# Performance work log

Measured on AMD Instinct MI355X. Metric: run time of the kernel, lower is better.

Reference implementation:

```python
import jax, jax.numpy as jnp
import numpy as np

B, C_ADD, H, W, NB = 4, 4, 496, 432, 50
SCALE = 0.8  # nonzero indices are multiplied by 0.8 in the original code


def setup_inputs() -> dict:
    key = jax.random.key(0)
    k1, k2, k3 = jax.random.split(key, 3)
    added_points = jax.random.normal(k1, (B, C_ADD, H, W), dtype=jnp.float32)
    original_points = jax.random.normal(k2, (B, C_ADD + 1, H, W), dtype=jnp.float32)
    # boxes: [x, y, z, dx, dy, dz, heading]; centers inside scaled grid extent
    u = jax.random.uniform(k3, (B, NB, 7), dtype=jnp.float32)
    cx = u[..., 0] * (H * SCALE)
    cy = u[..., 1] * (W * SCALE)
    cz = jnp.zeros_like(cx)
    dx = 2.0 + u[..., 3] * 6.0
    dy = 2.0 + u[..., 4] * 6.0
    dz = 1.0 + u[..., 5] * 2.0
    heading = (u[..., 6] - 0.5) * (2.0 * np.pi)
    boxes = jnp.stack([cx, cy, cz, dx, dy, dz, heading], axis=-1)
    return {"added_points": added_points, "original_points": original_points, "boxes": boxes}


def _points_in_boxes(points, boxes):
    # points: [P, 3]; boxes: [B, Nb, 7] -> bool [B, Nb, P]
    # OpenPCDet-style axis-aligned check in the box's rotated local frame.
    px = points[:, 0][None, None, :] - boxes[..., 0, None]  # [B, Nb, P]
    py = points[:, 1][None, None, :] - boxes[..., 1, None]
    pz = points[:, 2][None, None, :] - boxes[..., 2, None]
    c = jnp.cos(boxes[..., 6])[..., None]
    s = jnp.sin(boxes[..., 6])[..., None]
    lx = px * c + py * s
    ly = -px * s + py * c
    return (
        (jnp.abs(lx) <= boxes[..., 3, None] * 0.5)
        & (jnp.abs(ly) <= boxes[..., 4, None] * 0.5)
        & (jnp.abs(pz) <= boxes[..., 5, None] * 0.5)
    )


def reference(added_points, original_points, boxes):
    # collapse channels (original drops channel 0 of original_points)
    pred = jnp.sum(added_points, axis=1)            # [B, H, W]
    orig = jnp.sum(original_points[:, 1:], axis=1)  # [B, H, W]
    occ_pred = (pred != 0).reshape(B, 1, H * W)     # nonzero() -> occupancy mask
    occ_orig = (orig != 0).reshape(B, 1, H * W)
    # grid of (row*0.8, col*0.8, 0) points, shared across batch
    hh, ww = jnp.meshgrid(jnp.arange(H, dtype=jnp.float32),
                          jnp.arange(W, dtype=jnp.float32), indexing="ij")
    points = jnp.stack([hh * SCALE, ww * SCALE, jnp.zeros_like(hh)], axis=-1).reshape(H * W, 3)
    in_box = _points_in_boxes(points, boxes)        # [B, Nb, P] bool
    inter = jnp.sum(in_box & occ_pred & occ_orig, axis=-1).astype(jnp.float32)   # [B, Nb]
    union = jnp.sum(in_box & (occ_pred | occ_orig), axis=-1).astype(jnp.float32)
    iou = jnp.where(union > 0, inter / jnp.maximum(union, 1.0), 0.0)
    return jnp.sum(iou) / B
```

## Files before the change

kernel.cpp:

```cpp
#include <hip/hip_runtime.h>

#define BB     4
#define C_ADD  4
#define HH_    496
#define WW_    432
#define NB_    50
#define SCALE_ 0.8f

__global__ __launch_bounds__(64)
void points_iou_kernel(const float* __restrict__ added,
                       const float* __restrict__ orig,
                       const float* __restrict__ boxes,
                       float* __restrict__ out)
{
    const int HW = HH_ * WW_;
    const int blk = blockIdx.x;
    const int b   = blk / NB_;

    const float* bx = boxes + (size_t)blk * 7;
    const float cx = bx[0], cy = bx[1], cz = bx[2];
    const float dx = bx[3], dy = bx[4], dz = bx[5];
    const float hd = bx[6];
    const float c = cosf(hd), s = sinf(hd);

    const bool inz = fabsf(-cz) <= dz * 0.5f;

    const float ex = 0.5f * (dx * fabsf(c) + dy * fabsf(s));
    const float ey = 0.5f * (dx * fabsf(s) + dy * fabsf(c));

    int hmin = max(0,       (int)ceilf ((cx - ex) / SCALE_) - 1);
    int hmax = min(HH_ - 1, (int)floorf((cx + ex) / SCALE_) + 1);
    int wmin = max(0,       (int)ceilf ((cy - ey) / SCALE_) - 1);
    int wmax = min(WW_ - 1, (int)floorf((cy + ey) / SCALE_) + 1);
    const int nh = hmax - hmin + 1;
    const int nw = wmax - wmin + 1;

    int inter = 0, uni = 0;

    if (inz && nh > 0 && nw > 0) {
        const int ncell = nh * nw;
        const float* ab = added + (size_t)b * 4 * HW;
        const float* ob = orig  + (size_t)b * 5 * HW + HW;

        for (int idx = threadIdx.x; idx < ncell; idx += 64) {
            const int h = hmin + idx / nw;
            const int w = wmin + idx % nw;
            const float px = (float)h * SCALE_ - cx;
            const float py = (float)w * SCALE_ - cy;
            const float lx =  px * c + py * s;
            const float ly = -px * s + py * c;
            if (fabsf(lx) <= dx * 0.5f && fabsf(ly) <= dy * 0.5f) {
                const int p = h * WW_ + w;
                const float ps = ab[p] + ab[p + HW] + ab[p + 2 * HW] + ab[p + 3 * HW];
                const float os = ob[p] + ob[p + HW] + ob[p + 2 * HW] + ob[p + 3 * HW];
                const bool op = (ps != 0.0f);
                const bool oo = (os != 0.0f);
                inter += (op && oo) ? 1 : 0;
                uni   += (op || oo) ? 1 : 0;
            }
        }
    }

    #pragma unroll
    for (int off = 32; off > 0; off >>= 1) {
        inter += __shfl_down(inter, off);
        uni   += __shfl_down(uni,   off);
    }

    if (threadIdx.x == 0 && uni > 0) {
        atomicAdd(out, 0.25f * (float)inter / (float)uni);
    }
}

extern "C" void kernel_launch(void* const* d_in, const int* in_sizes, int n_in,
                              void* d_out, int out_size, void* d_ws, size_t ws_size,
                              hipStream_t stream) {
    const float* added = (const float*)d_in[0];
    const float* orig  = (const float*)d_in[1];
    const float* boxes = (const float*)d_in[2];
    float* out = (float*)d_out;

    hipMemsetAsync(out, 0, sizeof(float), stream);

    points_iou_kernel<<<BB * NB_, 64, 0, stream>>>(added, orig, boxes, out);
}
```

Before: 76.32 us.

## Widen per-box blocks to 256 threads and replace atomic/memset with reduce kernel

Each box block now runs four wavefronts instead of one, so the cells inside a box are covered with more memory-level parallelism. Per-wave partial counts are combined through shared memory. The memset plus float atomicAdd is replaced by per-block writes to workspace and a second single-block reduction kernel. This removes the memset and atomic contention but adds one extra kernel launch.

```diff
diff --git a/kernel.cpp b/kernel.cpp
--- a/kernel.cpp
+++ b/kernel.cpp
@@ -7,13 +7,16 @@
 #define NB_    50
 #define SCALE_ 0.8f
 
-__global__ __launch_bounds__(64)
-void points_iou_kernel(const float* __restrict__ added,
-                       const float* __restrict__ orig,
-                       const float* __restrict__ boxes,
-                       float* __restrict__ out)
+__global__ __launch_bounds__(256)
+void box_iou_kernel(const float* __restrict__ added,
+                    const float* __restrict__ orig,
+                    const float* __restrict__ boxes,
+                    float* __restrict__ ws)
 {
-    const int HW = HH_ * WW_;
+    __shared__ int s_inter[4];
+    __shared__ int s_uni[4];
+
+    const int HW  = HH_ * WW_;
     const int blk = blockIdx.x;
     const int b   = blk / NB_;
 
@@ -28,10 +31,10 @@
     const float ex = 0.5f * (dx * fabsf(c) + dy * fabsf(s));
     const float ey = 0.5f * (dx * fabsf(s) + dy * fabsf(c));
 
-    int hmin = max(0,       (int)ceilf ((cx - ex) / SCALE_) - 1);
-    int hmax = min(HH_ - 1, (int)floorf((cx + ex) / SCALE_) + 1);
-    int wmin = max(0,       (int)ceilf ((cy - ey) / SCALE_) - 1);
-    int wmax = min(WW_ - 1, (int)floorf((cy + ey) / SCALE_) + 1);
+    const int hmin = max(0,       (int)ceilf ((cx - ex) / SCALE_) - 1);
+    const int hmax = min(HH_ - 1, (int)floorf((cx + ex) / SCALE_) + 1);
+    const int wmin = max(0,       (int)ceilf ((cy - ey) / SCALE_) - 1);
+    const int wmax = min(WW_ - 1, (int)floorf((cy + ey) / SCALE_) + 1);
     const int nh = hmax - hmin + 1;
     const int nw = wmax - wmin + 1;
 
@@ -42,7 +45,7 @@
         const float* ab = added + (size_t)b * 4 * HW;
         const float* ob = orig  + (size_t)b * 5 * HW + HW;
 
-        for (int idx = threadIdx.x; idx < ncell; idx += 64) {
+        for (int idx = threadIdx.x; idx < ncell; idx += 256) {
             const int h = hmin + idx / nw;
             const int w = wmin + idx % nw;
             const float px = (float)h * SCALE_ - cx;
@@ -67,9 +70,25 @@
         uni   += __shfl_down(uni,   off);
     }
 
-    if (threadIdx.x == 0 && uni > 0) {
-        atomicAdd(out, 0.25f * (float)inter / (float)uni);
+    const int wid = threadIdx.x >> 6;
+    if ((threadIdx.x & 63) == 0) { s_inter[wid] = inter; s_uni[wid] = uni; }
+    __syncthreads();
+
+    if (threadIdx.x == 0) {
+        const int I = s_inter[0] + s_inter[1] + s_inter[2] + s_inter[3];
+        const int U = s_uni[0]   + s_uni[1]   + s_uni[2]   + s_uni[3];
+        ws[blk] = (U > 0) ? 0.25f * (float)I / (float)U : 0.0f;
     }
+}
+
+__global__ __launch_bounds__(64)
+void reduce_kernel(const float* __restrict__ ws, float* __restrict__ out)
+{
+    float v = 0.0f;
+    for (int i = threadIdx.x; i < BB * NB_; i += 64) v += ws[i];
+    #pragma unroll
+    for (int off = 32; off > 0; off >>= 1) v += __shfl_down(v, off);
+    if (threadIdx.x == 0) out[0] = v;
 }
 
 extern "C" void kernel_launch(void* const* d_in, const int* in_sizes, int n_in,
@@ -79,8 +98,8 @@
     const float* orig  = (const float*)d_in[1];
     const float* boxes = (const float*)d_in[2];
     float* out = (float*)d_out;
+    float* ws  = (float*)d_ws;
 
-    hipMemsetAsync(out, 0, sizeof(float), stream);
-
-    points_iou_kernel<<<BB * NB_, 64, 0, stream>>>(added, orig, boxes, out);
+    box_iou_kernel<<<BB * NB_, 256, 0, stream>>>(added, orig, boxes, ws);
+    reduce_kernel<<<1, 64, 0, stream>>>(ws, out);
 }
```

Measured after the change: 75.40 us. Within noise of the previous version (-1.2%).
